# Performance work log

Measured on AMD Instinct MI355X. Metric: run time of the kernel, lower is better.

## Reference

```python
import jax, jax.numpy as jnp
import numpy as np

WH, WW = 7, 7            # window size
NUM_HEADS = 4
PROMPT_LEN = 20          # PERTASK_LEN(5) * 4 tasks
DIM = 128
HEAD_DIM = DIM // NUM_HEADS
SCALE = HEAD_DIM ** -0.5


def _relative_position_index(wh, ww):
    coords = np.stack(np.meshgrid(np.arange(wh), np.arange(ww), indexing='ij'))  # [2,wh,ww]
    cf = coords.reshape(2, -1)                               # [2, wh*ww]
    rc = (cf[:, :, None] - cf[:, None, :]).transpose(1, 2, 0).astype(np.int64)
    rc[..., 0] += wh - 1
    rc[..., 1] += ww - 1
    rc[..., 0] *= 2 * ww - 1
    return rc.sum(-1)                                        # [wh*ww, wh*ww]

_REL_IDX = jnp.asarray(_relative_position_index(WH, WW))


def setup_inputs() -> dict:
    key = jax.random.key(0)
    ks = jax.random.split(key, 8)
    B, nW = 32, 64
    B_ = B * nW
    Nw = WH * WW
    return {
        'x': jax.random.normal(ks[0], (B_, Nw, DIM), jnp.float32),
        'spa_prompts': jax.random.normal(ks[1], (B, PROMPT_LEN, DIM), jnp.float32),
        'mask': jax.random.normal(ks[2], (nW, Nw, Nw), jnp.float32),
        'rel_bias_table': jax.random.normal(ks[3], ((2 * WH - 1) * (2 * WW - 1), NUM_HEADS), jnp.float32) * 0.02,
        'W_qkv': jax.random.normal(ks[4], (DIM, 3 * DIM), jnp.float32) * 0.02,
        'b_qkv': jax.random.normal(ks[5], (3 * DIM,), jnp.float32) * 0.02,
        'W_proj': jax.random.normal(ks[6], (DIM, DIM), jnp.float32) * 0.02,
        'b_proj': jax.random.normal(ks[7], (DIM,), jnp.float32) * 0.02,
    }


def reference(x, spa_prompts, mask, rel_bias_table, W_qkv, b_qkv, W_proj, b_proj):
    B_, Nw, C = x.shape
    B = spa_prompts.shape[0]
    nW = B_ // B
    P = PROMPT_LEN
    H = NUM_HEADS

    # replicate prompts per window and concat in front of window tokens
    prompts = jnp.broadcast_to(spa_prompts[:, None], (B, nW, P, C)).reshape(B_, P, C)
    xc = jnp.concatenate([prompts, x], axis=1)               # [B_, N, C]
    N = P + Nw

    qkv = xc @ W_qkv + b_qkv                                 # [B_, N, 3C]
    qkv = qkv.reshape(B_, N, 3, H, HEAD_DIM).transpose(2, 0, 3, 1, 4)
    q, k, v = qkv[0], qkv[1], qkv[2]                         # [B_, H, N, hd]

    attn_w = jnp.einsum('bhnd,bhmd->bhnm', q, k)             # unscaled q@k^T
    attn = attn_w * SCALE

    # relative position bias on the window-token sub-block
    bias = rel_bias_table[_REL_IDX]                          # [Nw, Nw, H]
    bias = bias.transpose(2, 0, 1)                           # [H, Nw, Nw]
    attn = attn.at[:, :, P:, P:].add(bias[None])

    # shifted-window mask on the same sub-block
    attn = attn.reshape(B, nW, H, N, N)
    attn = attn.at[:, :, :, P:, P:].add(mask[None, :, None])
    attn = attn.reshape(B_, H, N, N)

    attn = jax.nn.softmax(attn, axis=-1)

    out = jnp.einsum('bhnm,bhmd->bhnd', attn, v)             # [B_, H, N, hd]
    out = out.transpose(0, 2, 1, 3).reshape(B_, N, C)
    out = out @ W_proj + b_proj

    prompts_out, x_out = out[:, :P, :], out[:, P:, :]
    prompts_out = prompts_out.reshape(B, nW, P, C).mean(axis=1)
    ori_attn_weight = attn_w[:, :, :P, P:]                   # prompt->token raw scores
    return x_out, ori_attn_weight, prompts_out
```

## Files before the change

### kernel.cpp

```cpp
#include <hip/hip_runtime.h>
#include <hip/hip_bf16.h>

#define B_TOT   2048
#define BGRP    32
#define NW      64
#define NWIN    49
#define PLEN    20
#define NTOK    69
#define CDIM    128
#define NH      4
#define HD      32
#define SCALE_F 0.17677669529663687f

#define WIN_ROWS (B_TOT * NWIN)
#define PROMPT_ROWS (BGRP * PLEN)
#define TOT_ROWS (WIN_ROWS + PROMPT_ROWS)
#define PROJ_ROWS (B_TOT * NTOK)

typedef unsigned short ushort_t;
typedef __attribute__((ext_vector_type(8))) short bf16x8;
typedef __attribute__((ext_vector_type(4))) float f32x4;

__device__ __forceinline__ ushort_t f2b(float f) {
    union { float f; unsigned u; } v; v.f = f;
    unsigned r = v.u + 0x7FFFu + ((v.u >> 16) & 1u);
    return (ushort_t)(r >> 16);
}

__global__ __launch_bounds__(256) void convw_kernel(
    const float* __restrict__ Wqkv, const float* __restrict__ Wproj,
    ushort_t* __restrict__ Wtq, ushort_t* __restrict__ Wtp)
{
    int idx = blockIdx.x * 256 + threadIdx.x;
    if (idx < 384 * 128) {
        int n = idx >> 7, k = idx & 127;
        Wtq[idx] = f2b(Wqkv[k * 384 + n]);
    } else {
        int i = idx - 384 * 128;
        int n = i >> 7, k = i & 127;
        Wtp[i] = f2b(Wproj[k * 128 + n]);
    }
}

__global__ __launch_bounds__(256) void bm_kernel(
    const float* __restrict__ relb, const float* __restrict__ mask, float* __restrict__ bm)
{
    int idx = blockIdx.x * 256 + threadIdx.x;
    int jj = idx % 49; int t = idx / 49; int ii = t % 49; int wh = t / 49;
    int h = wh & 3, w = wh >> 2;
    int ridx = (ii / 7 - jj / 7 + 6) * 13 + (ii % 7 - jj % 7 + 6);
    bm[idx] = relb[ridx * NH + h] + mask[((size_t)w * 49 + ii) * 49 + jj];
}

__global__ __launch_bounds__(256) void qkv_kernel(
    const float* __restrict__ x, const float* __restrict__ prompts,
    const ushort_t* __restrict__ Wtq, const float* __restrict__ bqkv,
    ushort_t* __restrict__ q_win, ushort_t* __restrict__ k_win, ushort_t* __restrict__ v_win,
    ushort_t* __restrict__ q_p, ushort_t* __restrict__ k_p, ushort_t* __restrict__ v_p)
{
    __shared__ __align__(16) ushort_t As[128][136];
    __shared__ __align__(16) ushort_t Bs[128][136];
    const int m0 = blockIdx.x * 128;
    const int by = blockIdx.y;
    const int tid = threadIdx.x;

    for (int it = tid; it < 128 * 16; it += 256) {
        int r = it >> 4, ch = it & 15;
        int row = m0 + r;
        const float* src = (row < WIN_ROWS) ? x + (size_t)row * CDIM + ch * 8
                                            : prompts + (size_t)(row - WIN_ROWS) * CDIM + ch * 8;
        float4 v0 = *(const float4*)src;
        float4 v1 = *(const float4*)(src + 4);
        ushort_t tmp[8] = {f2b(v0.x), f2b(v0.y), f2b(v0.z), f2b(v0.w),
                           f2b(v1.x), f2b(v1.y), f2b(v1.z), f2b(v1.w)};
        *(uint4*)&As[r][ch * 8] = *(uint4*)tmp;
    }
    for (int it = tid; it < 128 * 16; it += 256) {
        int r = it >> 4, ch = it & 15;
        *(uint4*)&Bs[r][ch * 8] = *(const uint4*)(Wtq + ((size_t)(by * 128 + r)) * 128 + ch * 8);
    }
    __syncthreads();

    const int lane = tid & 63, wv = tid >> 6;
    const int wr = wv >> 1, wc = wv & 1;
    const int c = lane & 15, quad = lane >> 4;

    f32x4 acc[4][4];
#pragma unroll
    for (int i = 0; i < 4; i++)
#pragma unroll
        for (int j = 0; j < 4; j++) acc[i][j] = (f32x4){0.f, 0.f, 0.f, 0.f};

#pragma unroll
    for (int kc = 0; kc < 4; kc++) {
        bf16x8 a[4], b[4];
#pragma unroll
        for (int i = 0; i < 4; i++) a[i] = *(const bf16x8*)&As[wr * 64 + i * 16 + c][kc * 32 + quad * 8];
#pragma unroll
        for (int j = 0; j < 4; j++) b[j] = *(const bf16x8*)&Bs[wc * 64 + j * 16 + c][kc * 32 + quad * 8];
#pragma unroll
        for (int i = 0; i < 4; i++)
#pragma unroll
            for (int j = 0; j < 4; j++)
                acc[i][j] = __builtin_amdgcn_mfma_f32_16x16x32_bf16(a[i], b[j], acc[i][j], 0, 0, 0);
    }

    __syncthreads();
    ushort_t* Os = &As[0][0];
#pragma unroll
    for (int j = 0; j < 4; j++) {
        int col = wc * 64 + j * 16 + c;
        float bias = bqkv[by * 128 + col];
#pragma unroll
        for (int i = 0; i < 4; i++) {
            int rl = wr * 64 + i * 16 + quad * 4;
#pragma unroll
            for (int rr = 0; rr < 4; rr++)
                Os[(rl + rr) * 136 + col] = f2b(acc[i][j][rr] + bias);
        }
    }
    __syncthreads();

    ushort_t* dw = (by == 0) ? q_win : (by == 1) ? k_win : v_win;
    ushort_t* dp = (by == 0) ? q_p   : (by == 1) ? k_p   : v_p;
    for (int it = tid; it < 128 * 16; it += 256) {
        int r = it >> 4, ch = it & 15;
        int row = m0 + r;
        uint4 val = *(uint4*)&Os[r * 136 + ch * 8];
        if (row < WIN_ROWS) *(uint4*)&dw[(size_t)row * CDIM + ch * 8] = val;
        else                *(uint4*)&dp[(size_t)(row - WIN_ROWS) * CDIM + ch * 8] = val;
    }
}

__global__ __launch_bounds__(256, 3) void attn_kernel(
    const ushort_t* __restrict__ q_win, const ushort_t* __restrict__ k_win, const ushort_t* __restrict__ v_win,
    const ushort_t* __restrict__ q_p, const ushort_t* __restrict__ k_p, const ushort_t* __restrict__ v_p,
    const float* __restrict__ bm,
    ushort_t* __restrict__ attn_out, float* __restrict__ ori_w)
{
    __shared__ __align__(16) ushort_t Vt[4][32][104];
    __shared__ __align__(16) ushort_t Ps[4][16][104];

    const int b = blockIdx.x;
    const int bb = b >> 6;
    const int w = b & 63;
    const int tid = threadIdx.x;

    for (int it = tid; it < 64 * 2; it += 256) {
        int row = it >> 1, half = it & 1;
        *(uint4*)&Ps[row >> 4][row & 15][80 + half * 8] = (uint4){0u, 0u, 0u, 0u};
    }
    for (int it = tid; it < 128 * 27; it += 256) {
        int d = it / 27, cc = 69 + it % 27;
        Vt[d >> 5][d & 31][cc] = 0;
    }
    for (int it = tid; it < 69 * 16; it += 256) {
        int n = it >> 4, ch = it & 15;
        const ushort_t* vb = (n < PLEN) ? v_p + ((size_t)bb * PLEN + n) * CDIM
                                        : v_win + ((size_t)b * NWIN + (n - PLEN)) * CDIM;
        uint4 vv = *(const uint4*)(vb + ch * 8);
        ushort_t tmp[8]; *(uint4*)tmp = vv;
        int hh = ch >> 2, dbase = (ch & 3) * 8;
#pragma unroll
        for (int i = 0; i < 8; i++) Vt[hh][dbase + i][n] = tmp[i];
    }
    __syncthreads();

    const int lane = tid & 63, h = tid >> 6;
    const int c = lane & 15, quad = lane >> 4;
    const int dsl = h * HD + quad * 8;

    bf16x8 kf[5];
#pragma unroll
    for (int j = 0; j < 5; j++) {
        int n = j * 16 + c; if (n > 68) n = 68;
        const ushort_t* kb = (n < PLEN) ? k_p + ((size_t)bb * PLEN + n) * CDIM
                                        : k_win + ((size_t)b * NWIN + (n - PLEN)) * CDIM;
        kf[j] = *(const bf16x8*)(kb + dsl);
    }
    bf16x8 vf[2][3];
#pragma unroll
    for (int dt = 0; dt < 2; dt++)
#pragma unroll
        for (int kc = 0; kc < 3; kc++)
            vf[dt][kc] = *(const bf16x8*)&Vt[h][dt * 16 + c][kc * 32 + quad * 8];

    const float* bmw = bm + (size_t)(w * NH + h) * (49 * 49);

    for (int itile = 0; itile < 5; itile++) {
        int nq = itile * 16 + c; if (nq > 68) nq = 68;
        const ushort_t* qb = (nq < PLEN) ? q_p + ((size_t)bb * PLEN + nq) * CDIM
                                         : q_win + ((size_t)b * NWIN + (nq - PLEN)) * CDIM;
        bf16x8 qf = *(const bf16x8*)(qb + dsl);

        f32x4 s[5];
#pragma unroll
        for (int j = 0; j < 5; j++)
            s[j] = __builtin_amdgcn_mfma_f32_16x16x32_bf16(qf, kf[j], (f32x4){0.f, 0.f, 0.f, 0.f}, 0, 0, 0);

        const int mbase = itile * 16 + quad * 4;

        if (mbase < 20) {
#pragma unroll
            for (int j = 1; j < 5; j++) {
                int col = j * 16 + c;
                if (col >= 20 && col < 69) {
#pragma unroll
                    for (int rr = 0; rr < 4; rr++) {
                        int m = mbase + rr;
                        if (m < 20)
                            ori_w[(((size_t)b * NH + h) * PLEN + m) * NWIN + (col - 20)] = s[j][rr];
                    }
                }
            }
        }
#pragma unroll
        for (int j = 0; j < 5; j++) {
            int col = j * 16 + c;
#pragma unroll
            for (int rr = 0; rr < 4; rr++) {
                int m = mbase + rr;
                float v;
                if (col >= 69) v = -1e30f;
                else {
                    v = s[j][rr] * SCALE_F;
                    if (m >= 20 && m < 69 && col >= 20)
                        v += bmw[(m - 20) * 49 + (col - 20)];
                }
                s[j][rr] = v;
            }
        }
#pragma unroll
        for (int rr = 0; rr < 4; rr++) {
            float mx = fmaxf(fmaxf(fmaxf(s[0][rr], s[1][rr]), fmaxf(s[2][rr], s[3][rr])), s[4][rr]);
            mx = fmaxf(mx, __shfl_xor(mx, 1));
            mx = fmaxf(mx, __shfl_xor(mx, 2));
            mx = fmaxf(mx, __shfl_xor(mx, 4));
            mx = fmaxf(mx, __shfl_xor(mx, 8));
            float e0 = __expf(s[0][rr] - mx), e1 = __expf(s[1][rr] - mx), e2 = __expf(s[2][rr] - mx);
            float e3 = __expf(s[3][rr] - mx), e4 = __expf(s[4][rr] - mx);
            float sum = e0 + e1 + e2 + e3 + e4;
            sum += __shfl_xor(sum, 1);
            sum += __shfl_xor(sum, 2);
            sum += __shfl_xor(sum, 4);
            sum += __shfl_xor(sum, 8);
            float inv = 1.f / sum;
            int mrow = quad * 4 + rr;
            Ps[h][mrow][c]      = f2b(e0 * inv);
            Ps[h][mrow][16 + c] = f2b(e1 * inv);
            Ps[h][mrow][32 + c] = f2b(e2 * inv);
            Ps[h][mrow][48 + c] = f2b(e3 * inv);
            Ps[h][mrow][64 + c] = f2b(e4 * inv);
        }
#pragma unroll
        for (int dt = 0; dt < 2; dt++) {
            f32x4 o = {0.f, 0.f, 0.f, 0.f};
#pragma unroll
            for (int kc = 0; kc < 3; kc++) {
                bf16x8 pa = *(const bf16x8*)&Ps[h][c][kc * 32 + quad * 8];
                o = __builtin_amdgcn_mfma_f32_16x16x32_bf16(pa, vf[dt][kc], o, 0, 0, 0);
            }
#pragma unroll
            for (int rr = 0; rr < 4; rr++) {
                int m = mbase + rr;
                if (m < 69)
                    attn_out[((size_t)b * NTOK + m) * CDIM + h * HD + dt * 16 + c] = f2b(o[rr]);
            }
        }
    }
}

__global__ __launch_bounds__(256) void proj_kernel(
    const ushort_t* __restrict__ attn_out, const ushort_t* __restrict__ Wtp,
    const float* __restrict__ bproj,
    float* __restrict__ x_out, float* __restrict__ promptproj)
{
    __shared__ __align__(16) char smem[128 * 136 * 4];
    ushort_t (*As)[136] = (ushort_t(*)[136])smem;
    ushort_t (*Bs)[136] = (ushort_t(*)[136])(smem + 128 * 136 * 2);
    float (*Osf)[136] = (float(*)[136])smem;

    const int m0 = blockIdx.x * 128;
    const int tid = threadIdx.x;

    for (int it = tid; it < 128 * 16; it += 256) {
        int r = it >> 4, ch = it & 15;
        *(uint4*)&As[r][ch * 8] = *(const uint4*)(attn_out + (size_t)(m0 + r) * CDIM + ch * 8);
    }
    for (int it = tid; it < 128 * 16; it += 256) {
        int r = it >> 4, ch = it & 15;
        *(uint4*)&Bs[r][ch * 8] = *(const uint4*)(Wtp + (size_t)r * 128 + ch * 8);
    }
    __syncthreads();

    const int lane = tid & 63, wv = tid >> 6;
    const int wr = wv >> 1, wc = wv & 1;
    const int c = lane & 15, quad = lane >> 4;

    f32x4 acc[4][4];
#pragma unroll
    for (int i = 0; i < 4; i++)
#pragma unroll
        for (int j = 0; j < 4; j++) acc[i][j] = (f32x4){0.f, 0.f, 0.f, 0.f};

#pragma unroll
    for (int kc = 0; kc < 4; kc++) {
        bf16x8 a[4], b[4];
#pragma unroll
        for (int i = 0; i < 4; i++) a[i] = *(const bf16x8*)&As[wr * 64 + i * 16 + c][kc * 32 + quad * 8];
#pragma unroll
        for (int j = 0; j < 4; j++) b[j] = *(const bf16x8*)&Bs[wc * 64 + j * 16 + c][kc * 32 + quad * 8];
#pragma unroll
        for (int i = 0; i < 4; i++)
#pragma unroll
            for (int j = 0; j < 4; j++)
                acc[i][j] = __builtin_amdgcn_mfma_f32_16x16x32_bf16(a[i], b[j], acc[i][j], 0, 0, 0);
    }

    __syncthreads();
#pragma unroll
    for (int j = 0; j < 4; j++) {
        int col = wc * 64 + j * 16 + c;
        float bias = bproj[col];
#pragma unroll
        for (int i = 0; i < 4; i++) {
            int rl = wr * 64 + i * 16 + quad * 4;
#pragma unroll
            for (int rr = 0; rr < 4; rr++)
                Osf[rl + rr][col] = acc[i][j][rr] + bias;
        }
    }
    __syncthreads();

    for (int it = tid; it < 128 * 32; it += 256) {
        int r = it >> 5, ch = it & 31;
        float4 val = *(float4*)&Osf[r][ch * 4];
        int row = m0 + r;
        int bidx = row / NTOK, n = row - bidx * NTOK;
        if (n >= PLEN)
            *(float4*)&x_out[((size_t)bidx * NWIN + (n - PLEN)) * CDIM + ch * 4] = val;
        else
            *(float4*)&promptproj[((size_t)bidx * PLEN + n) * CDIM + ch * 4] = val;
    }
}

__global__ __launch_bounds__(256) void mean_kernel(
    const float* __restrict__ promptproj, float* __restrict__ prompts_out)
{
    int idx = blockIdx.x * 256 + threadIdx.x;
    if (idx >= BGRP * PLEN * CDIM) return;
    int c = idx & 127;
    int p = (idx >> 7) % PLEN;
    int bb = idx / (PLEN * CDIM);
    size_t base = (((size_t)bb * NW) * PLEN + p) * CDIM + c;
    float s = 0.f;
    for (int w = 0; w < NW; w++) s += promptproj[base + (size_t)w * (PLEN * CDIM)];
    prompts_out[idx] = s * (1.f / 64.f);
}

extern "C" void kernel_launch(void* const* d_in, const int* in_sizes, int n_in,
                              void* d_out, int out_size, void* d_ws, size_t ws_size,
                              hipStream_t stream)
{
    const float* x       = (const float*)d_in[0];
    const float* prompts = (const float*)d_in[1];
    const float* mask    = (const float*)d_in[2];
    const float* relb    = (const float*)d_in[3];
    const float* Wqkv    = (const float*)d_in[4];
    const float* bqkv    = (const float*)d_in[5];
    const float* Wproj   = (const float*)d_in[6];
    const float* bproj   = (const float*)d_in[7];

    float* out = (float*)d_out;
    float* x_out       = out;
    float* ori_w       = out + (size_t)B_TOT * NWIN * CDIM;
    float* prompts_out = ori_w + (size_t)B_TOT * NH * PLEN * NWIN;

    char* wsb = (char*)d_ws;
    size_t off = 0;
    const size_t winQKV = (size_t)WIN_ROWS * CDIM;
    const size_t pQKV   = (size_t)PROMPT_ROWS * CDIM;
    ushort_t* q_win = (ushort_t*)(wsb + off); off += winQKV * 2;
    ushort_t* k_win = (ushort_t*)(wsb + off); off += winQKV * 2;
    ushort_t* v_win = (ushort_t*)(wsb + off); off += winQKV * 2;
    ushort_t* q_p   = (ushort_t*)(wsb + off); off += pQKV * 2;
    ushort_t* k_p   = (ushort_t*)(wsb + off); off += pQKV * 2;
    ushort_t* v_p   = (ushort_t*)(wsb + off); off += pQKV * 2;
    ushort_t* attn_o = (ushort_t*)(wsb + off); off += (size_t)PROJ_ROWS * CDIM * 2;
    float* promptproj = (float*)(wsb + off); off += (size_t)B_TOT * PLEN * CDIM * 4;
    float* bm = (float*)(wsb + off); off += (size_t)NW * NH * 49 * 49 * 4;
    ushort_t* Wtq = (ushort_t*)(wsb + off); off += 384 * 128 * 2;
    ushort_t* Wtp = (ushort_t*)(wsb + off); off += 128 * 128 * 2;

    convw_kernel<<<256, 256, 0, stream>>>(Wqkv, Wproj, Wtq, Wtp);
    bm_kernel<<<(NW * NH * 49 * 49) / 256, 256, 0, stream>>>(relb, mask, bm);
    qkv_kernel<<<dim3(TOT_ROWS / 128, 3), 256, 0, stream>>>(x, prompts, Wtq, bqkv,
                                                            q_win, k_win, v_win, q_p, k_p, v_p);
    attn_kernel<<<B_TOT, 256, 0, stream>>>(q_win, k_win, v_win, q_p, k_p, v_p,
                                           bm, attn_o, ori_w);
    proj_kernel<<<PROJ_ROWS / 128, 256, 0, stream>>>(attn_o, Wtp, bproj, x_out, promptproj);
    mean_kernel<<<(BGRP * PLEN * CDIM + 255) / 256, 256, 0, stream>>>(promptproj, prompts_out);
}
```

Before: 269.7 us.

## Reuse converted x tile across QKV chunks, swizzle attention LDS, pad bias to 80x80

The QKV kernel now loads and converts each 128-row x tile once and loops over the Q, K and V weight chunks inside the block. Before, each of three y-blocks reloaded and re-converted the fp32 input. The attention kernel's Vt and Ps shared arrays are widened to 128 columns with an XOR swizzle to reduce LDS bank conflicts. The bias+mask table is precomputed as a padded 80x80 per window/head, including -1e30 for padding columns, so the score epilogue becomes a single unconditional fma. The trade-offs are a larger bias table to read (6400 vs 2401 floats per window/head), more shared memory, and a third of the QKV grid size.

New measurement: 254.0 us. 5.8% less time.

```diff
diff --git a/kernel.cpp b/kernel.cpp
--- a/kernel.cpp
+++ b/kernel.cpp
@@ -27,6 +27,8 @@
     return (ushort_t)(r >> 16);
 }
 
+__device__ __forceinline__ int swz(int row, int col) { return col ^ ((row & 7) << 3); }
+
 __global__ __launch_bounds__(256) void convw_kernel(
     const float* __restrict__ Wqkv, const float* __restrict__ Wproj,
     ushort_t* __restrict__ Wtq, ushort_t* __restrict__ Wtp)
@@ -42,14 +44,21 @@
     }
 }
 
-__global__ __launch_bounds__(256) void bm_kernel(
-    const float* __restrict__ relb, const float* __restrict__ mask, float* __restrict__ bm)
+__global__ __launch_bounds__(256) void bm80_kernel(
+    const float* __restrict__ relb, const float* __restrict__ mask, float* __restrict__ bm80)
 {
     int idx = blockIdx.x * 256 + threadIdx.x;
-    int jj = idx % 49; int t = idx / 49; int ii = t % 49; int wh = t / 49;
+    int col = idx % 80; int t = idx / 80; int row = t % 80; int wh = t / 80;
     int h = wh & 3, w = wh >> 2;
-    int ridx = (ii / 7 - jj / 7 + 6) * 13 + (ii % 7 - jj % 7 + 6);
-    bm[idx] = relb[ridx * NH + h] + mask[((size_t)w * 49 + ii) * 49 + jj];
+    float v;
+    if (col >= 69)      v = (row < 69) ? -1e30f : 0.f;
+    else if (row < 20 || col < 20 || row >= 69) v = 0.f;
+    else {
+        int ii = row - 20, jj = col - 20;
+        int ridx = (ii / 7 - jj / 7 + 6) * 13 + (ii % 7 - jj % 7 + 6);
+        v = relb[ridx * NH + h] + mask[((size_t)w * 49 + ii) * 49 + jj];
+    }
+    bm80[idx] = v;
 }
 
 __global__ __launch_bounds__(256) void qkv_kernel(
@@ -61,7 +70,6 @@
     __shared__ __align__(16) ushort_t As[128][136];
     __shared__ __align__(16) ushort_t Bs[128][136];
     const int m0 = blockIdx.x * 128;
-    const int by = blockIdx.y;
     const int tid = threadIdx.x;
 
     for (int it = tid; it < 128 * 16; it += 256) {
@@ -75,84 +83,98 @@
                            f2b(v1.x), f2b(v1.y), f2b(v1.z), f2b(v1.w)};
         *(uint4*)&As[r][ch * 8] = *(uint4*)tmp;
     }
-    for (int it = tid; it < 128 * 16; it += 256) {
-        int r = it >> 4, ch = it & 15;
-        *(uint4*)&Bs[r][ch * 8] = *(const uint4*)(Wtq + ((size_t)(by * 128 + r)) * 128 + ch * 8);
-    }
     __syncthreads();
 
     const int lane = tid & 63, wv = tid >> 6;
     const int wr = wv >> 1, wc = wv & 1;
     const int c = lane & 15, quad = lane >> 4;
 
-    f32x4 acc[4][4];
-#pragma unroll
-    for (int i = 0; i < 4; i++)
-#pragma unroll
-        for (int j = 0; j < 4; j++) acc[i][j] = (f32x4){0.f, 0.f, 0.f, 0.f};
-
-#pragma unroll
-    for (int kc = 0; kc < 4; kc++) {
-        bf16x8 a[4], b[4];
-#pragma unroll
-        for (int i = 0; i < 4; i++) a[i] = *(const bf16x8*)&As[wr * 64 + i * 16 + c][kc * 32 + quad * 8];
-#pragma unroll
-        for (int j = 0; j < 4; j++) b[j] = *(const bf16x8*)&Bs[wc * 64 + j * 16 + c][kc * 32 + quad * 8];
+    bf16x8 af[4][4];
+#pragma unroll
+    for (int kc = 0; kc < 4; kc++)
 #pragma unroll
         for (int i = 0; i < 4; i++)
+            af[kc][i] = *(const bf16x8*)&As[wr * 64 + i * 16 + c][kc * 32 + quad * 8];
+
+    for (int chunk = 0; chunk < 3; chunk++) {
+        for (int it = tid; it < 128 * 16; it += 256) {
+            int r = it >> 4, ch = it & 15;
+            *(uint4*)&Bs[r][ch * 8] =
+                *(const uint4*)(Wtq + ((size_t)(chunk * 128 + r)) * 128 + ch * 8);
+        }
+        __syncthreads();
+
+        f32x4 acc[4][4];
+#pragma unroll
+        for (int i = 0; i < 4; i++)
+#pragma unroll
+            for (int j = 0; j < 4; j++) acc[i][j] = (f32x4){0.f, 0.f, 0.f, 0.f};
+
+#pragma unroll
+        for (int kc = 0; kc < 4; kc++) {
+            bf16x8 b[4];
 #pragma unroll
             for (int j = 0; j < 4; j++)
-                acc[i][j] = __builtin_amdgcn_mfma_f32_16x16x32_bf16(a[i], b[j], acc[i][j], 0, 0, 0);
-    }
-
-    __syncthreads();
-    ushort_t* Os = &As[0][0];
-#pragma unroll
-    for (int j = 0; j < 4; j++) {
-        int col = wc * 64 + j * 16 + c;
-        float bias = bqkv[by * 128 + col];
-#pragma unroll
-        for (int i = 0; i < 4; i++) {
-            int rl = wr * 64 + i * 16 + quad * 4;
-#pragma unroll
-            for (int rr = 0; rr < 4; rr++)
-                Os[(rl + rr) * 136 + col] = f2b(acc[i][j][rr] + bias);
-        }
-    }
-    __syncthreads();
-
-    ushort_t* dw = (by == 0) ? q_win : (by == 1) ? k_win : v_win;
-    ushort_t* dp = (by == 0) ? q_p   : (by == 1) ? k_p   : v_p;
-    for (int it = tid; it < 128 * 16; it += 256) {
-        int r = it >> 4, ch = it & 15;
-        int row = m0 + r;
-        uint4 val = *(uint4*)&Os[r * 136 + ch * 8];
-        if (row < WIN_ROWS) *(uint4*)&dw[(size_t)row * CDIM + ch * 8] = val;
-        else                *(uint4*)&dp[(size_t)(row - WIN_ROWS) * CDIM + ch * 8] = val;
+                b[j] = *(const bf16x8*)&Bs[wc * 64 + j * 16 + c][kc * 32 + quad * 8];
+#pragma unroll
+            for (int i = 0; i < 4; i++)
+#pragma unroll
+                for (int j = 0; j < 4; j++)
+                    acc[i][j] = __builtin_amdgcn_mfma_f32_16x16x32_bf16(af[kc][i], b[j], acc[i][j], 0, 0, 0);
+        }
+        __syncthreads();
+
+        ushort_t* Os = &Bs[0][0];
+#pragma unroll
+        for (int j = 0; j < 4; j++) {
+            int col = wc * 64 + j * 16 + c;
+            float bias = bqkv[chunk * 128 + col];
+#pragma unroll
+            for (int i = 0; i < 4; i++) {
+                int rl = wr * 64 + i * 16 + quad * 4;
+#pragma unroll
+                for (int rr = 0; rr < 4; rr++)
+                    Os[(rl + rr) * 136 + col] = f2b(acc[i][j][rr] + bias);
+            }
+        }
+        __syncthreads();
+
+        ushort_t* dw = (chunk == 0) ? q_win : (chunk == 1) ? k_win : v_win;
+        ushort_t* dp = (chunk == 0) ? q_p   : (chunk == 1) ? k_p   : v_p;
+        for (int it = tid; it < 128 * 16; it += 256) {
+            int r = it >> 4, ch = it & 15;
+            int row = m0 + r;
+            uint4 val = *(uint4*)&Os[r * 136 + ch * 8];
+            if (row < WIN_ROWS) *(uint4*)&dw[(size_t)row * CDIM + ch * 8] = val;
+            else                *(uint4*)&dp[(size_t)(row - WIN_ROWS) * CDIM + ch * 8] = val;
+        }
+        __syncthreads();
     }
 }
 
 __global__ __launch_bounds__(256, 3) void attn_kernel(
     const ushort_t* __restrict__ q_win, const ushort_t* __restrict__ k_win, const ushort_t* __restrict__ v_win,
     const ushort_t* __restrict__ q_p, const ushort_t* __restrict__ k_p, const ushort_t* __restrict__ v_p,
-    const float* __restrict__ bm,
+    const float* __restrict__ bm80,
     ushort_t* __restrict__ attn_out, float* __restrict__ ori_w)
 {
-    __shared__ __align__(16) ushort_t Vt[4][32][104];
-    __shared__ __align__(16) ushort_t Ps[4][16][104];
+    __shared__ __align__(16) ushort_t Vt[4][32][128];
+    __shared__ __align__(16) ushort_t Ps[4][16][128];
 
     const int b = blockIdx.x;
     const int bb = b >> 6;
     const int w = b & 63;
     const int tid = threadIdx.x;
 
-    for (int it = tid; it < 64 * 2; it += 256) {
-        int row = it >> 1, half = it & 1;
-        *(uint4*)&Ps[row >> 4][row & 15][80 + half * 8] = (uint4){0u, 0u, 0u, 0u};
-    }
-    for (int it = tid; it < 128 * 27; it += 256) {
-        int d = it / 27, cc = 69 + it % 27;
-        Vt[d >> 5][d & 31][cc] = 0;
+    for (int it = tid; it < 4 * 32 * 27; it += 256) {
+        int hh = it / (32 * 27), rem = it % (32 * 27);
+        int d = rem / 27, cc = 69 + rem % 27;
+        Vt[hh][d][swz(d, cc)] = 0;
+    }
+    for (int it = tid; it < 4 * 16 * 16; it += 256) {
+        int hh = it >> 8, rem = it & 255;
+        int r = rem >> 4, cc = 80 + (rem & 15);
+        Ps[hh][r][swz(r, cc)] = 0;
     }
     for (int it = tid; it < 69 * 16; it += 256) {
         int n = it >> 4, ch = it & 15;
@@ -162,13 +184,17 @@
         ushort_t tmp[8]; *(uint4*)tmp = vv;
         int hh = ch >> 2, dbase = (ch & 3) * 8;
 #pragma unroll
-        for (int i = 0; i < 8; i++) Vt[hh][dbase + i][n] = tmp[i];
+        for (int i = 0; i < 8; i++) {
+            int d = dbase + i;
+            Vt[hh][d][swz(d, n)] = tmp[i];
+        }
     }
     __syncthreads();
 
     const int lane = tid & 63, h = tid >> 6;
     const int c = lane & 15, quad = lane >> 4;
     const int dsl = h * HD + quad * 8;
+    const int xk_rd = (c & 7) << 3;
 
     bf16x8 kf[5];
 #pragma unroll
@@ -183,9 +209,9 @@
     for (int dt = 0; dt < 2; dt++)
 #pragma unroll
         for (int kc = 0; kc < 3; kc++)
-            vf[dt][kc] = *(const bf16x8*)&Vt[h][dt * 16 + c][kc * 32 + quad * 8];
-
-    const float* bmw = bm + (size_t)(w * NH + h) * (49 * 49);
+            vf[dt][kc] = *(const bf16x8*)&Vt[h][dt * 16 + c][(kc * 32 + quad * 8) ^ xk_rd];
+
+    const float* bmw = bm80 + (size_t)(w * NH + h) * 6400;
 
     for (int itile = 0; itile < 5; itile++) {
         int nq = itile * 16 + c; if (nq > 68) nq = 68;
@@ -216,18 +242,10 @@
         }
 #pragma unroll
         for (int j = 0; j < 5; j++) {
-            int col = j * 16 + c;
 #pragma unroll
             for (int rr = 0; rr < 4; rr++) {
                 int m = mbase + rr;
-                float v;
-                if (col >= 69) v = -1e30f;
-                else {
-                    v = s[j][rr] * SCALE_F;
-                    if (m >= 20 && m < 69 && col >= 20)
-                        v += bmw[(m - 20) * 49 + (col - 20)];
-                }
-                s[j][rr] = v;
+                s[j][rr] = fmaf(s[j][rr], SCALE_F, bmw[m * 80 + j * 16 + c]);
             }
         }
 #pragma unroll
@@ -246,18 +264,19 @@
             sum += __shfl_xor(sum, 8);
             float inv = 1.f / sum;
             int mrow = quad * 4 + rr;
-            Ps[h][mrow][c]      = f2b(e0 * inv);
-            Ps[h][mrow][16 + c] = f2b(e1 * inv);
-            Ps[h][mrow][32 + c] = f2b(e2 * inv);
-            Ps[h][mrow][48 + c] = f2b(e3 * inv);
-            Ps[h][mrow][64 + c] = f2b(e4 * inv);
+            int xw = (mrow & 7) << 3;
+            Ps[h][mrow][(c) ^ xw]      = f2b(e0 * inv);
+            Ps[h][mrow][(16 + c) ^ xw] = f2b(e1 * inv);
+            Ps[h][mrow][(32 + c) ^ xw] = f2b(e2 * inv);
+            Ps[h][mrow][(48 + c) ^ xw] = f2b(e3 * inv);
+            Ps[h][mrow][(64 + c) ^ xw] = f2b(e4 * inv);
         }
 #pragma unroll
         for (int dt = 0; dt < 2; dt++) {
             f32x4 o = {0.f, 0.f, 0.f, 0.f};
 #pragma unroll
             for (int kc = 0; kc < 3; kc++) {
-                bf16x8 pa = *(const bf16x8*)&Ps[h][c][kc * 32 + quad * 8];
+                bf16x8 pa = *(const bf16x8*)&Ps[h][c][(kc * 32 + quad * 8) ^ xk_rd];
                 o = __builtin_amdgcn_mfma_f32_16x16x32_bf16(pa, vf[dt][kc], o, 0, 0, 0);
             }
 #pragma unroll
@@ -388,16 +407,16 @@
     ushort_t* v_p   = (ushort_t*)(wsb + off); off += pQKV * 2;
     ushort_t* attn_o = (ushort_t*)(wsb + off); off += (size_t)PROJ_ROWS * CDIM * 2;
     float* promptproj = (float*)(wsb + off); off += (size_t)B_TOT * PLEN * CDIM * 4;
-    float* bm = (float*)(wsb + off); off += (size_t)NW * NH * 49 * 49 * 4;
+    float* bm80 = (float*)(wsb + off); off += (size_t)NW * NH * 80 * 80 * 4;
     ushort_t* Wtq = (ushort_t*)(wsb + off); off += 384 * 128 * 2;
     ushort_t* Wtp = (ushort_t*)(wsb + off); off += 128 * 128 * 2;
 
     convw_kernel<<<256, 256, 0, stream>>>(Wqkv, Wproj, Wtq, Wtp);
-    bm_kernel<<<(NW * NH * 49 * 49) / 256, 256, 0, stream>>>(relb, mask, bm);
-    qkv_kernel<<<dim3(TOT_ROWS / 128, 3), 256, 0, stream>>>(x, prompts, Wtq, bqkv,
-                                                            q_win, k_win, v_win, q_p, k_p, v_p);
+    bm80_kernel<<<(NW * NH * 80 * 80) / 256, 256, 0, stream>>>(relb, mask, bm80);
+    qkv_kernel<<<TOT_ROWS / 128, 256, 0, stream>>>(x, prompts, Wtq, bqkv,
+                                                   q_win, k_win, v_win, q_p, k_p, v_p);
     attn_kernel<<<B_TOT, 256, 0, stream>>>(q_win, k_win, v_win, q_p, k_p, v_p,
-                                           bm, attn_o, ori_w);
+                                           bm80, attn_o, ori_w);
     proj_kernel<<<PROJ_ROWS / 128, 256, 0, stream>>>(attn_o, Wtp, bproj, x_out, promptproj);
     mean_kernel<<<(BGRP * PLEN * CDIM + 255) / 256, 256, 0, stream>>>(promptproj, prompts_out);
 }
```
